# Kernel tuning notes

Hardware: AMD Instinct MI355X
Metric: run time of the kernel (lower is better)

The kernel has to match this reference:

```python
import jax, jax.numpy as jnp
import numpy as np

T, B, E, H, V, L = 64, 64, 512, 1024, 10000, 2


def setup_inputs() -> dict:
    key = jax.random.key(0)
    ks = jax.random.split(key, 24)
    k = 1.0 / np.sqrt(H)
    u = lambda kk, shape, s: jax.random.uniform(kk, shape, jnp.float32, -s, s)
    return {
        "inputs": jax.random.randint(ks[0], (T, B), 0, V, dtype=jnp.int32),
        "hidden": jnp.zeros((L, B, H), jnp.float32),
        "emb": u(ks[1], (V, E), 0.1),
        "Wr0": u(ks[2], (H, E), k),
        "Wz0": u(ks[3], (H, E), k),
        "Wh0": u(ks[4], (H, E), k),
        "WrR": u(ks[5], (L - 1, H, H), k),
        "WzR": u(ks[6], (L - 1, H, H), k),
        "WhR": u(ks[7], (L - 1, H, H), k),
        "brR": u(ks[8], (L - 1, H), k),
        "bzR": u(ks[9], (L - 1, H), k),
        "bhR": u(ks[10], (L - 1, H), k),
        "Ur": u(ks[11], (L, H, H), k),
        "Uz": u(ks[12], (L, H, H), k),
        "Uh": u(ks[13], (L, H, H), k),
        "bur": u(ks[14], (L, H), k),
        "buz": u(ks[15], (L, H), k),
        "buh": u(ks[16], (L, H), k),
        "Wout": u(ks[17], (V, H), 0.1),
        "bout": jnp.zeros((V,), jnp.float32),
    }


def reference(inputs, hidden, emb, Wr0, Wz0, Wh0, WrR, WzR, WhR, brR, bzR, bhR,
              Ur, Uz, Uh, bur, buz, buh, Wout, bout):
    num_layers = hidden.shape[0]
    x_emb = emb[inputs]  # [T, B, E]

    def step(h_prev, x_t):  # h_prev [L,B,H], x_t [B,E]
        x = x_t
        hs = []
        for l in range(num_layers):
            if l == 0:
                rx = x @ Wr0.T  # layer-0 W* have no bias
                zx = x @ Wz0.T
                hx = x @ Wh0.T
            else:
                rx = x @ WrR[l - 1].T + brR[l - 1]
                zx = x @ WzR[l - 1].T + bzR[l - 1]
                hx = x @ WhR[l - 1].T + bhR[l - 1]
            hl = h_prev[l]
            r = jax.nn.sigmoid(rx + hl @ Ur[l].T + bur[l])
            z = jax.nn.sigmoid(zx + hl @ Uz[l].T + buz[l])
            h_tilda = jnp.tanh(hx + (r * hl) @ Uh[l].T + buh[l])
            h_new = (1.0 - z) * hl + z * h_tilda
            hs.append(h_new)
            x = h_new
        logits_t = x @ Wout.T + bout  # [B, V]
        return jnp.stack(hs), logits_t

    h_final, logits = jax.lax.scan(step, hidden, x_emb)
    return logits, h_final  # logits [T,B,V], h_final [L,B,H]
```

## Files before the change

kernel.cpp:

```cpp
#include <hip/hip_runtime.h>
#include <hip/hip_bf16.h>

#define T_ 64
#define B_ 64
#define E_ 512
#define H_ 1024
#define V_ 10000
#define TB 4096
#define BH 65536

typedef unsigned short u16;
typedef unsigned int u32;
typedef unsigned long long u64;
typedef __attribute__((ext_vector_type(8))) short short8v;
typedef __attribute__((ext_vector_type(4))) float f32x4;

__device__ inline f32x4 mfma_bf16(short8v a, short8v b, f32x4 c) {
  return __builtin_amdgcn_mfma_f32_16x16x32_bf16(a, b, c, 0, 0, 0);
}

__device__ inline u16 f2bf(float f) {
  unsigned u = __float_as_uint(f);
  unsigned r = (u + 0x7fffu + ((u >> 16) & 1u)) >> 16;
  return (u16)r;
}
__device__ inline float bf2f(u16 h) { return __uint_as_float(((unsigned)h) << 16); }


__global__ void k_prep(const float* __restrict__ Wr0, const float* __restrict__ Wz0,
                       const float* __restrict__ Wh0, const float* __restrict__ Ur,
                       const float* __restrict__ Uz, const float* __restrict__ Uh,
                       const float* __restrict__ WrR, const float* __restrict__ WzR,
                       const float* __restrict__ WhR, const float* __restrict__ Wout,
                       const int* __restrict__ idx, const float* __restrict__ emb,
                       const float* __restrict__ bur, const float* __restrict__ buz,
                       const float* __restrict__ buh, const float* __restrict__ brR,
                       const float* __restrict__ bzR, const float* __restrict__ bhR,
                       const float* __restrict__ hidden,
                       u16* __restrict__ W0cat, u16* __restrict__ U0cat,
                       u16* __restrict__ U1W, u16* __restrict__ Woutb,
                       u16* __restrict__ x_bf, float* __restrict__ bias0,
                       float* __restrict__ bias1, u16* __restrict__ h0P,
                       u16* __restrict__ h1P) {
  const int HE = H_ * E_;
  const int HH = H_ * H_;
  const size_t n0 = 3u * (size_t)HE;
  const size_t n1 = n0 + 3u * (size_t)HH;
  const size_t n2 = n1 + 3072u * 2048u;
  const size_t n3 = n2 + (size_t)V_ * H_;
  const size_t n4 = n3 + (size_t)TB * E_;
  const size_t n5 = n4 + 3072;
  const size_t n6 = n5 + 65536;
  size_t i = (size_t)blockIdx.x * 256 + threadIdx.x;
  const size_t stride = (size_t)gridDim.x * 256;
  for (; i < n6; i += stride) {
    if (i < n0) {
      int g = (int)(i >> 19), off = (int)(i & (HE - 1));
      const float* s = g == 0 ? Wr0 : (g == 1 ? Wz0 : Wh0);
      W0cat[i] = f2bf(s[off]);
    } else if (i < n1) {
      size_t j = i - n0;
      int g = (int)(j >> 20), off = (int)(j & (HH - 1));
      const float* s = g == 0 ? Ur : (g == 1 ? Uz : Uh);
      U0cat[j] = f2bf(s[off]);
    } else if (i < n2) {
      size_t k = i - n1;
      int row = (int)(k >> 11), kk = (int)(k & 2047);
      int g = row >> 10, jj = row & 1023;
      const float* su = g == 0 ? Ur : (g == 1 ? Uz : Uh);
      const float* sw = g == 0 ? WrR : (g == 1 ? WzR : WhR);
      float v = (kk < 1024) ? su[(size_t)HH + (size_t)jj * 1024 + kk]
                            : sw[(size_t)jj * 1024 + (kk - 1024)];
      U1W[k] = f2bf(v);
    } else if (i < n3) {
      size_t m = i - n2;
      Woutb[m] = f2bf(Wout[m]);
    } else if (i < n4) {
      size_t j = i - n3;
      int row = (int)(j >> 9), e = (int)(j & 511);
      x_bf[j] = f2bf(emb[(size_t)idx[row] * E_ + e]);
    } else if (i < n5) {
      int j = (int)(i - n4);
      int seg = j >> 10, col = j & 1023;
      float b0, b1;
      if (seg == 0)      { b0 = bur[col]; b1 = brR[col] + bur[H_ + col]; }
      else if (seg == 1) { b0 = buz[col]; b1 = bzR[col] + buz[H_ + col]; }
      else               { b0 = buh[col]; b1 = bhR[col] + buh[H_ + col]; }
      bias0[j] = b0; bias1[j] = b1;
    } else {
      int j = (int)(i - n5);
      int row = j >> 10, c = j & 1023;
      int dst = ((c >> 4) << 10) + (row << 4) + (c & 15);
      h0P[dst] = f2bf(hidden[j]);
      h1P[dst] = f2bf(hidden[BH + j]);
    }
  }
}


__global__ __launch_bounds__(256, 2) void k_gemmX(const u16* __restrict__ A,
                                                  const u16* __restrict__ Wt,
                                                  const float* __restrict__ bias,
                                                  u16* __restrict__ XP) {
  const int m0 = blockIdx.x * 128, n0 = blockIdx.y * 128;
  const int wid = threadIdx.x >> 6, lane = threadIdx.x & 63;
  const int wm = wid >> 1, wn = wid & 1;
  const int lrow = lane & 15, lk = (lane >> 4) * 8;
  f32x4 acc[4][4] = {};
  const u16* Ab = A + (size_t)(m0 + wm * 64 + lrow) * 512 + lk;
  const u16* Wb = Wt + (size_t)(n0 + wn * 64 + lrow) * 512 + lk;
  for (int ks = 0; ks < 512; ks += 32) {
    short8v a[4], b[4];
#pragma unroll
    for (int f = 0; f < 4; f++) a[f] = *(const short8v*)(Ab + (size_t)f * 16 * 512 + ks);
#pragma unroll
    for (int f = 0; f < 4; f++) b[f] = *(const short8v*)(Wb + (size_t)f * 16 * 512 + ks);
#pragma unroll
    for (int i = 0; i < 4; i++)
#pragma unroll
      for (int j = 0; j < 4; j++) acc[i][j] = mfma_bf16(a[i], b[j], acc[i][j]);
  }
  const int drow0 = (lane >> 4) * 4, dcol = lane & 15;
#pragma unroll
  for (int i = 0; i < 4; i++)
#pragma unroll
    for (int j = 0; j < 4; j++) {
      int col = n0 + wn * 64 + j * 16 + dcol;
      float bv = bias[col];
      int g = col >> 10, cg = (col & 1023) >> 4, cc = col & 15;
#pragma unroll
      for (int v = 0; v < 4; v++) {
        int row = m0 + wm * 64 + i * 16 + drow0 + v;
        int t = row >> 6, rr = row & 63;
        XP[(((size_t)t * 64 + cg) * 64 + rr) * 48 + g * 16 + cc] = f2bf(acc[i][j][v] + bv);
      }
    }
}


__global__ __launch_bounds__(256, 2) void k_gemmL(const u16* __restrict__ AP,
                                                  const u16* __restrict__ Wt,
                                                  const float* __restrict__ bias,
                                                  float* __restrict__ C) {
  const int xcd = blockIdx.x & 7, idx = blockIdx.x >> 3;
  const int nt = xcd * 10 + (idx % 10);
  const int mt = idx / 10;
  if (nt >= 79) return;
  const int m0 = mt * 128, n0 = nt * 128;
  const int wid = threadIdx.x >> 6, lane = threadIdx.x & 63;
  const int wm = wid >> 1, wn = wid & 1;
  const int lrow = lane & 15, lk = (lane >> 4) * 8;
  const int lkb = lk >> 4, lkc = lk & 15;
  f32x4 acc[4][4] = {};
  const int rowhi = (m0 + wm * 64) >> 6;
  const u16* Ab = AP + (size_t)rowhi * BH + (size_t)lkb * 1024 + lrow * 16 + lkc;
  const u16* Wb = Wt + (size_t)(n0 + wn * 64 + lrow) * 1024 + lk;
  bool nvalid[4];
#pragma unroll
  for (int f = 0; f < 4; f++) nvalid[f] = (n0 + wn * 64 + f * 16 + lrow) < V_;
  const short8v zv = {};
  for (int ks = 0; ks < 1024; ks += 32) {
    short8v a[4], b[4];
#pragma unroll
    for (int f = 0; f < 4; f++) a[f] = *(const short8v*)(Ab + ks * 64 + f * 256);
#pragma unroll
    for (int f = 0; f < 4; f++)
      b[f] = nvalid[f] ? *(const short8v*)(Wb + (size_t)f * 16 * 1024 + ks) : zv;
#pragma unroll
    for (int i = 0; i < 4; i++)
#pragma unroll
      for (int j = 0; j < 4; j++) acc[i][j] = mfma_bf16(a[i], b[j], acc[i][j]);
  }
  const int drow0 = (lane >> 4) * 4, dcol = lane & 15;
#pragma unroll
  for (int i = 0; i < 4; i++)
#pragma unroll
    for (int j = 0; j < 4; j++) {
      int col = n0 + wn * 64 + j * 16 + dcol;
      if (col >= V_) continue;
      float bv = bias[col];
#pragma unroll
      for (int v = 0; v < 4; v++) {
        int row = m0 + wm * 64 + i * 16 + drow0 + v;
        C[(size_t)row * V_ + col] = acc[i][j][v] + bv;
      }
    }
}


__device__ inline void pollall(const int* slots, int tgt) {
  const int lane = threadIdx.x & 63;
  const int* p = slots + lane * 32;
  for (;;) {
    int v = __hip_atomic_load(p, __ATOMIC_RELAXED, __HIP_MEMORY_SCOPE_AGENT);
    if (__all(v >= tgt)) break;
    __builtin_amdgcn_s_sleep(1);
  }
}

__global__ __launch_bounds__(256, 1) void k_recur(
    const u16* __restrict__ U0, const u16* __restrict__ U1W,
    const u16* __restrict__ XP, const float* __restrict__ bias1,
    const float* __restrict__ hidden,
    u16* __restrict__ h0P, u16* __restrict__ h1P,
    u16* __restrict__ r0P, u16* __restrict__ r1P,
    int* __restrict__ flags, float* __restrict__ hfin) {
  __shared__ __align__(16) u16 wlds[65536];

  const int tid = threadIdx.x, gbid = blockIdx.x;
  const int lay = gbid >> 6;
  const int cg = gbid & 63;
  const int jr = cg * 16;
  const int wid = tid >> 6, lane = tid & 63;
  const int lrow = lane & 15, lk = (lane >> 4) * 8;
  const int lk3 = lk >> 3, x7 = lrow & 7;
  const int drow0 = (lane >> 4) * 4, dcol = lane & 15;
  const int abase = (lk >> 4) * 1024 + (wid * 16 + lrow) * 16 + (lk & 15);
  const int KLS = lay ? 11 : 10;
  int* f0s = flags;
  int* f1s = flags + 2048;
  int* myslot = (lay ? f1s : f0s) + cg * 32;

  {
    const u16* Wg = lay ? U1W : U0;
    const int lCPR = lay ? 8 : 7;
    const int NG = lay ? 2 : 3;
    const int total = NG << (4 + lCPR);
    const int KL = 1 << KLS;
    for (int idx = tid; idx < total; idx += 256) {
      int r16 = idx >> lCPR;
      int ch = idx & ((1 << lCPR) - 1);
      int g = r16 >> 4, r = r16 & 15;
      short8v v = *(const short8v*)(Wg + (size_t)((g << 10) + jr + r) * KL + (ch << 3));
      *(short8v*)&wlds[((size_t)r16 << KLS) + ((ch ^ (r & 7)) << 3)] = v;
    }
  }
  __syncthreads();

  const int lbR = lrow << KLS;
  const int lbZ = (16 + lrow) << KLS;
  const int lbH = (32 + lrow) << KLS;
  const u16* Whg = U1W + (size_t)(2048 + jr + lrow) * 2048 + lk;
  const int orow = wid * 16 + drow0;

  float hreg[4];
#pragma unroll
  for (int v = 0; v < 4; v++)
    hreg[v] = hidden[(size_t)lay * BH + (size_t)(orow + v) * 1024 + jr + dcol];

  if (!lay) {
    float xr[4], xz[4], xh[4];
    {
      const u16* xb = XP + (((size_t)0 * 64 + cg) * 64 + orow) * 48 + dcol;
#pragma unroll
      for (int v = 0; v < 4; v++) {
        xr[v] = bf2f(xb[v * 48]);
        xz[v] = bf2f(xb[v * 48 + 16]);
        xh[v] = bf2f(xb[v * 48 + 32]);
      }
    }
    for (int t = 0; t < T_; t++) {
      float zreg[4];
      if (t) { if (wid == 0) pollall(f0s, 2 * t); __syncthreads(); }
      short8v av[32];
      {
        const u16* Ab = h0P + (size_t)t * BH + abase;
#pragma unroll
        for (int i = 0; i < 32; i++) av[i] = *(const short8v*)(Ab + i * 2048);
      }
      f32x4 ar = {};
#pragma unroll
      for (int i = 0; i < 32; i++) {
        const int sw = (((i * 4) + lk3) ^ x7) << 3;
        ar = mfma_bf16(av[i], *(short8v*)&wlds[lbR + sw], ar);
      }
      u16* rtile = r0P + (size_t)t * BH + (size_t)cg * 1024;
#pragma unroll
      for (int v = 0; v < 4; v++) {
        float r = 1.f / (1.f + __expf(-(ar[v] + xr[v])));
        u16 me = f2bf(r * hreg[v]);
        int oth = __shfl_xor((int)me, 1);
        if (!(dcol & 1)) {
          u32 pk = (u32)me | ((u32)(u16)oth << 16);
          __hip_atomic_store((u32*)(rtile + (orow + v) * 16 + dcol), pk,
                             __ATOMIC_RELAXED, __HIP_MEMORY_SCOPE_AGENT);
        }
      }
      asm volatile("s_waitcnt vmcnt(0)" ::: "memory");
      __syncthreads();
      if (tid == 0)
        __hip_atomic_store(myslot, 2 * t + 1, __ATOMIC_RELAXED, __HIP_MEMORY_SCOPE_AGENT);
      f32x4 az = {};
#pragma unroll
      for (int i = 0; i < 32; i++) {
        const int sw = (((i * 4) + lk3) ^ x7) << 3;
        az = mfma_bf16(av[i], *(short8v*)&wlds[lbZ + sw], az);
      }
#pragma unroll
      for (int v = 0; v < 4; v++) zreg[v] = 1.f / (1.f + __expf(-(az[v] + xz[v])));
      float nxr[4], nxz[4], nxh[4];
      {
        int tn = t + 1 < T_ ? t + 1 : T_ - 1;
        const u16* xb = XP + (((size_t)tn * 64 + cg) * 64 + orow) * 48 + dcol;
#pragma unroll
        for (int v = 0; v < 4; v++) {
          nxr[v] = bf2f(xb[v * 48]);
          nxz[v] = bf2f(xb[v * 48 + 16]);
          nxh[v] = bf2f(xb[v * 48 + 32]);
        }
      }
      if (wid == 0) pollall(f0s, 2 * t + 1);
      __syncthreads();
      f32x4 ah = {};
      {
        const u16* Abr = r0P + (size_t)t * BH + abase;
        short8v avr[32];
#pragma unroll
        for (int i = 0; i < 32; i++) avr[i] = *(const short8v*)(Abr + i * 2048);
#pragma unroll
        for (int i = 0; i < 32; i++) {
          const int sw = (((i * 4) + lk3) ^ x7) << 3;
          ah = mfma_bf16(avr[i], *(short8v*)&wlds[lbH + sw], ah);
        }
      }
      u16* htile = h0P + (size_t)(t + 1) * BH + (size_t)cg * 1024;
#pragma unroll
      for (int v = 0; v < 4; v++) {
        float th = tanhf(ah[v] + xh[v]);
        float hn = (1.f - zreg[v]) * hreg[v] + zreg[v] * th;
        hreg[v] = hn;
        u16 me = f2bf(hn);
        int oth = __shfl_xor((int)me, 1);
        if (!(dcol & 1)) {
          u32 pk = (u32)me | ((u32)(u16)oth << 16);
          __hip_atomic_store((u32*)(htile + (orow + v) * 16 + dcol), pk,
                             __ATOMIC_RELAXED, __HIP_MEMORY_SCOPE_AGENT);
        }
        if (t == T_ - 1)
          hfin[(size_t)(orow + v) * 1024 + jr + dcol] = hn;
      }
      asm volatile("s_waitcnt vmcnt(0)" ::: "memory");
      __syncthreads();
      if (tid == 0)
        __hip_atomic_store(myslot, 2 * t + 2, __ATOMIC_RELAXED, __HIP_MEMORY_SCOPE_AGENT);
#pragma unroll
      for (int v = 0; v < 4; v++) { xr[v] = nxr[v]; xz[v] = nxz[v]; xh[v] = nxh[v]; }
    }
  } else {
    float bR = bias1[jr + dcol];
    float bZ = bias1[1024 + jr + dcol];
    float bH = bias1[2048 + jr + dcol];
    if (wid == 0) pollall(f0s, 2);
    __syncthreads();
    for (int t = 0; t < T_; t++) {
      float zreg[4];
      const u16* Ab0 = h0P + (size_t)(t + 1) * BH + abase;
      f32x4 ar = {}, az = {};
      short8v av0[32];
#pragma unroll
      for (int i = 0; i < 32; i++) av0[i] = *(const short8v*)(Ab0 + i * 2048);
#pragma unroll
      for (int i = 0; i < 32; i++) {
        const int sw = ((128 + i * 4 + lk3) ^ x7) << 3;
        ar = mfma_bf16(av0[i], *(short8v*)&wlds[lbR + sw], ar);
        az = mfma_bf16(av0[i], *(short8v*)&wlds[lbZ + sw], az);
      }
      if (wid == 0) {
        if (t) pollall(f1s, 2 * t);
      } else if (wid == 1) {
        int tgt = 2 * (t + 2);
        pollall(f0s, tgt > 2 * T_ ? 2 * T_ : tgt);
      }
      __syncthreads();
      short8v av1[32];
      {
        const u16* Ab1 = h1P + (size_t)t * BH + abase;
#pragma unroll
        for (int i = 0; i < 32; i++) av1[i] = *(const short8v*)(Ab1 + i * 2048);
      }
#pragma unroll
      for (int i = 0; i < 32; i++) {
        const int sw = ((i * 4 + lk3) ^ x7) << 3;
        ar = mfma_bf16(av1[i], *(short8v*)&wlds[lbR + sw], ar);
      }
      u16* rtile = r1P + (size_t)t * BH + (size_t)cg * 1024;
#pragma unroll
      for (int v = 0; v < 4; v++) {
        float r = 1.f / (1.f + __expf(-(ar[v] + bR)));
        u16 me = f2bf(r * hreg[v]);
        int oth = __shfl_xor((int)me, 1);
        if (!(dcol & 1)) {
          u32 pk = (u32)me | ((u32)(u16)oth << 16);
          __hip_atomic_store((u32*)(rtile + (orow + v) * 16 + dcol), pk,
                             __ATOMIC_RELAXED, __HIP_MEMORY_SCOPE_AGENT);
        }
      }
      asm volatile("s_waitcnt vmcnt(0)" ::: "memory");
      __syncthreads();
      if (tid == 0)
        __hip_atomic_store(myslot, 2 * t + 1, __ATOMIC_RELAXED, __HIP_MEMORY_SCOPE_AGENT);
#pragma unroll
      for (int i = 0; i < 32; i++) {
        const int sw = ((i * 4 + lk3) ^ x7) << 3;
        az = mfma_bf16(av1[i], *(short8v*)&wlds[lbZ + sw], az);
      }
#pragma unroll
      for (int v = 0; v < 4; v++) zreg[v] = 1.f / (1.f + __expf(-(az[v] + bZ)));
      f32x4 ah = {};
#pragma unroll
      for (int i = 0; i < 32; i++)
        ah = mfma_bf16(av0[i], *(const short8v*)(Whg + 1024 + i * 32), ah);
      if (wid == 0) pollall(f1s, 2 * t + 1);
      __syncthreads();
      {
        const u16* Abr = r1P + (size_t)t * BH + abase;
        short8v avr[32];
#pragma unroll
        for (int i = 0; i < 32; i++) avr[i] = *(const short8v*)(Abr + i * 2048);
#pragma unroll
        for (int i = 0; i < 32; i++)
          ah = mfma_bf16(avr[i], *(const short8v*)(Whg + i * 32), ah);
      }
      u16* htile = h1P + (size_t)(t + 1) * BH + (size_t)cg * 1024;
#pragma unroll
      for (int v = 0; v < 4; v++) {
        float th = tanhf(ah[v] + bH);
        float hn = (1.f - zreg[v]) * hreg[v] + zreg[v] * th;
        hreg[v] = hn;
        u16 me = f2bf(hn);
        int oth = __shfl_xor((int)me, 1);
        if (!(dcol & 1)) {
          u32 pk = (u32)me | ((u32)(u16)oth << 16);
          __hip_atomic_store((u32*)(htile + (orow + v) * 16 + dcol), pk,
                             __ATOMIC_RELAXED, __HIP_MEMORY_SCOPE_AGENT);
        }
        if (t == T_ - 1)
          hfin[(size_t)BH + (size_t)(orow + v) * 1024 + jr + dcol] = hn;
      }
      asm volatile("s_waitcnt vmcnt(0)" ::: "memory");
      __syncthreads();
      if (tid == 0)
        __hip_atomic_store(myslot, 2 * t + 2, __ATOMIC_RELAXED, __HIP_MEMORY_SCOPE_AGENT);
    }
  }
}


extern "C" void kernel_launch(void* const* d_in, const int* in_sizes, int n_in,
                              void* d_out, int out_size, void* d_ws, size_t ws_size,
                              hipStream_t stream) {
  const int* inputs = (const int*)d_in[0];
  const float* hidden = (const float*)d_in[1];
  const float* emb = (const float*)d_in[2];
  const float* Wr0 = (const float*)d_in[3];
  const float* Wz0 = (const float*)d_in[4];
  const float* Wh0 = (const float*)d_in[5];
  const float* WrR = (const float*)d_in[6];
  const float* WzR = (const float*)d_in[7];
  const float* WhR = (const float*)d_in[8];
  const float* brR = (const float*)d_in[9];
  const float* bzR = (const float*)d_in[10];
  const float* bhR = (const float*)d_in[11];
  const float* Ur = (const float*)d_in[12];
  const float* Uz = (const float*)d_in[13];
  const float* Uh = (const float*)d_in[14];
  const float* bur = (const float*)d_in[15];
  const float* buz = (const float*)d_in[16];
  const float* buh = (const float*)d_in[17];
  const float* Wout = (const float*)d_in[18];
  const float* bout = (const float*)d_in[19];
  float* out = (float*)d_out;

  char* ws = (char*)d_ws;
  size_t off = 0;
  auto alloc = [&](size_t bytes) -> void* {
    void* p = ws + off;
    off += (bytes + 255) & ~(size_t)255;
    return p;
  };
  u16* x_bf  = (u16*)alloc((size_t)TB * E_ * 2);
  u16* W0cat = (u16*)alloc((size_t)3072 * 512 * 2);
  u16* U0cat = (u16*)alloc((size_t)3072 * 1024 * 2);
  u16* U1W   = (u16*)alloc((size_t)3072 * 2048 * 2);
  u16* Woutb = (u16*)alloc((size_t)V_ * H_ * 2);
  float* bias0 = (float*)alloc(3072 * 4);
  float* bias1 = (float*)alloc(3072 * 4);
  u16* XP    = (u16*)alloc((size_t)TB * 3072 * 2);
  u16* h0P   = (u16*)alloc((size_t)(T_ + 1) * BH * 2);
  u16* h1P   = (u16*)alloc((size_t)(T_ + 1) * BH * 2);
  u16* r0P   = (u16*)alloc((size_t)T_ * BH * 2);
  u16* r1P   = (u16*)alloc((size_t)T_ * BH * 2);
  int* flags = (int*)alloc(32768);
  (void)ws_size; (void)in_sizes; (void)n_in; (void)out_size;

  hipMemsetAsync(flags, 0, 32768, stream);

  k_prep<<<2048, 256, 0, stream>>>(Wr0, Wz0, Wh0, Ur, Uz, Uh, WrR, WzR, WhR, Wout,
                                   inputs, emb, bur, buz, buh, brR, bzR, bhR, hidden,
                                   W0cat, U0cat, U1W, Woutb, x_bf, bias0, bias1,
                                   h0P, h1P);
  k_gemmX<<<dim3(32, 24), 256, 0, stream>>>(x_bf, W0cat, bias0, XP);
  k_recur<<<128, 256, 0, stream>>>(U0cat, U1W, XP, bias1, hidden, h0P, h1P,
                                   r0P, r1P, flags, out + (size_t)TB * V_);
  k_gemmL<<<2560, 256, 0, stream>>>(h1P + BH, Woutb, bout, out);
}
```

Before: 1.382 ms.

## Fuse output projection GEMM into recurrent kernel with flag-gated tiles

Removes the separate output-logits GEMM launch and appends its tiles as extra blocks of the persistent recurrence kernel. Each GEMM block polls the layer-1 progress flags until the two timesteps covering its 128 rows are finished, then computes them, so the vocabulary projection overlaps the sequential recurrence. The added blocks share the device with the 128 recurrence blocks, which rely on co-residency for their spin-wait barriers. This risks scheduling or deadlock issues if GEMM blocks take the slots the recurrence blocks need, and their polling and memory traffic may slow the critical path.

```diff
diff --git a/kernel.cpp b/kernel.cpp
--- a/kernel.cpp
+++ b/kernel.cpp
@@ -138,63 +138,14 @@
 }
 
 
-__global__ __launch_bounds__(256, 2) void k_gemmL(const u16* __restrict__ AP,
-                                                  const u16* __restrict__ Wt,
-                                                  const float* __restrict__ bias,
-                                                  float* __restrict__ C) {
-  const int xcd = blockIdx.x & 7, idx = blockIdx.x >> 3;
-  const int nt = xcd * 10 + (idx % 10);
-  const int mt = idx / 10;
-  if (nt >= 79) return;
-  const int m0 = mt * 128, n0 = nt * 128;
-  const int wid = threadIdx.x >> 6, lane = threadIdx.x & 63;
-  const int wm = wid >> 1, wn = wid & 1;
-  const int lrow = lane & 15, lk = (lane >> 4) * 8;
-  const int lkb = lk >> 4, lkc = lk & 15;
-  f32x4 acc[4][4] = {};
-  const int rowhi = (m0 + wm * 64) >> 6;
-  const u16* Ab = AP + (size_t)rowhi * BH + (size_t)lkb * 1024 + lrow * 16 + lkc;
-  const u16* Wb = Wt + (size_t)(n0 + wn * 64 + lrow) * 1024 + lk;
-  bool nvalid[4];
-#pragma unroll
-  for (int f = 0; f < 4; f++) nvalid[f] = (n0 + wn * 64 + f * 16 + lrow) < V_;
-  const short8v zv = {};
-  for (int ks = 0; ks < 1024; ks += 32) {
-    short8v a[4], b[4];
-#pragma unroll
-    for (int f = 0; f < 4; f++) a[f] = *(const short8v*)(Ab + ks * 64 + f * 256);
-#pragma unroll
-    for (int f = 0; f < 4; f++)
-      b[f] = nvalid[f] ? *(const short8v*)(Wb + (size_t)f * 16 * 1024 + ks) : zv;
-#pragma unroll
-    for (int i = 0; i < 4; i++)
-#pragma unroll
-      for (int j = 0; j < 4; j++) acc[i][j] = mfma_bf16(a[i], b[j], acc[i][j]);
-  }
-  const int drow0 = (lane >> 4) * 4, dcol = lane & 15;
-#pragma unroll
-  for (int i = 0; i < 4; i++)
-#pragma unroll
-    for (int j = 0; j < 4; j++) {
-      int col = n0 + wn * 64 + j * 16 + dcol;
-      if (col >= V_) continue;
-      float bv = bias[col];
-#pragma unroll
-      for (int v = 0; v < 4; v++) {
-        int row = m0 + wm * 64 + i * 16 + drow0 + v;
-        C[(size_t)row * V_ + col] = acc[i][j][v] + bv;
-      }
-    }
-}
-
-
+template <int SLP>
 __device__ inline void pollall(const int* slots, int tgt) {
   const int lane = threadIdx.x & 63;
   const int* p = slots + lane * 32;
   for (;;) {
     int v = __hip_atomic_load(p, __ATOMIC_RELAXED, __HIP_MEMORY_SCOPE_AGENT);
     if (__all(v >= tgt)) break;
-    __builtin_amdgcn_s_sleep(1);
+    __builtin_amdgcn_s_sleep(SLP);
   }
 }
 
@@ -204,21 +155,72 @@
     const float* __restrict__ hidden,
     u16* __restrict__ h0P, u16* __restrict__ h1P,
     u16* __restrict__ r0P, u16* __restrict__ r1P,
+    const u16* __restrict__ Woutb, const float* __restrict__ bout,
+    float* __restrict__ out,
     int* __restrict__ flags, float* __restrict__ hfin) {
   __shared__ __align__(16) u16 wlds[65536];
 
   const int tid = threadIdx.x, gbid = blockIdx.x;
+  const int wid = tid >> 6, lane = tid & 63;
+  const int lrow = lane & 15, lk = (lane >> 4) * 8;
+  const int drow0 = (lane >> 4) * 4, dcol = lane & 15;
+  int* f0s = flags;
+  int* f1s = flags + 2048;
+
+  if (gbid >= 128) {
+    const int w = gbid - 128;
+    const int mt = w / 79, nt = w % 79;
+    const int m0 = mt * 128, n0 = nt * 128;
+    const int wm = wid >> 1, wn = wid & 1;
+    const int lkb = lk >> 4, lkc = lk & 15;
+    if (wid == 0) {
+      int tgt = 4 * mt + 4;
+      pollall<32>(f1s, tgt > 2 * T_ ? 2 * T_ : tgt);
+    }
+    __syncthreads();
+    const u16* AP = h1P + BH;
+    f32x4 acc[4][4] = {};
+    const int rowhi = (m0 + wm * 64) >> 6;
+    const u16* Ab = AP + (size_t)rowhi * BH + (size_t)lkb * 1024 + lrow * 16 + lkc;
+    const u16* Wb = Woutb + (size_t)(n0 + wn * 64 + lrow) * 1024 + lk;
+    bool nvalid[4];
+#pragma unroll
+    for (int f = 0; f < 4; f++) nvalid[f] = (n0 + wn * 64 + f * 16 + lrow) < V_;
+    const short8v zv = {};
+    for (int ks = 0; ks < 1024; ks += 32) {
+      short8v a[4], b[4];
+#pragma unroll
+      for (int f = 0; f < 4; f++) a[f] = *(const short8v*)(Ab + ks * 64 + f * 256);
+#pragma unroll
+      for (int f = 0; f < 4; f++)
+        b[f] = nvalid[f] ? *(const short8v*)(Wb + (size_t)f * 16 * 1024 + ks) : zv;
+#pragma unroll
+      for (int i = 0; i < 4; i++)
+#pragma unroll
+        for (int j = 0; j < 4; j++) acc[i][j] = mfma_bf16(a[i], b[j], acc[i][j]);
+    }
+#pragma unroll
+    for (int i = 0; i < 4; i++)
+#pragma unroll
+      for (int j = 0; j < 4; j++) {
+        int col = n0 + wn * 64 + j * 16 + dcol;
+        if (col >= V_) continue;
+        float bv = bout[col];
+#pragma unroll
+        for (int v = 0; v < 4; v++) {
+          int row = m0 + wm * 64 + i * 16 + drow0 + v;
+          out[(size_t)row * V_ + col] = acc[i][j][v] + bv;
+        }
+      }
+    return;
+  }
+
   const int lay = gbid >> 6;
   const int cg = gbid & 63;
   const int jr = cg * 16;
-  const int wid = tid >> 6, lane = tid & 63;
-  const int lrow = lane & 15, lk = (lane >> 4) * 8;
   const int lk3 = lk >> 3, x7 = lrow & 7;
-  const int drow0 = (lane >> 4) * 4, dcol = lane & 15;
   const int abase = (lk >> 4) * 1024 + (wid * 16 + lrow) * 16 + (lk & 15);
   const int KLS = lay ? 11 : 10;
-  int* f0s = flags;
-  int* f1s = flags + 2048;
   int* myslot = (lay ? f1s : f0s) + cg * 32;
 
   {
@@ -261,7 +263,7 @@
     }
     for (int t = 0; t < T_; t++) {
       float zreg[4];
-      if (t) { if (wid == 0) pollall(f0s, 2 * t); __syncthreads(); }
+      if (t) { if (wid == 0) pollall<1>(f0s, 2 * t); __syncthreads(); }
       short8v av[32];
       {
         const u16* Ab = h0P + (size_t)t * BH + abase;
@@ -309,7 +311,7 @@
           nxh[v] = bf2f(xb[v * 48 + 32]);
         }
       }
-      if (wid == 0) pollall(f0s, 2 * t + 1);
+      if (wid == 0) pollall<1>(f0s, 2 * t + 1);
       __syncthreads();
       f32x4 ah = {};
       {
@@ -350,7 +352,7 @@
     float bR = bias1[jr + dcol];
     float bZ = bias1[1024 + jr + dcol];
     float bH = bias1[2048 + jr + dcol];
-    if (wid == 0) pollall(f0s, 2);
+    if (wid == 0) pollall<1>(f0s, 2);
     __syncthreads();
     for (int t = 0; t < T_; t++) {
       float zreg[4];
@@ -366,10 +368,10 @@
         az = mfma_bf16(av0[i], *(short8v*)&wlds[lbZ + sw], az);
       }
       if (wid == 0) {
-        if (t) pollall(f1s, 2 * t);
+        if (t) pollall<1>(f1s, 2 * t);
       } else if (wid == 1) {
         int tgt = 2 * (t + 2);
-        pollall(f0s, tgt > 2 * T_ ? 2 * T_ : tgt);
+        pollall<1>(f0s, tgt > 2 * T_ ? 2 * T_ : tgt);
       }
       __syncthreads();
       short8v av1[32];
@@ -410,7 +412,7 @@
 #pragma unroll
       for (int i = 0; i < 32; i++)
         ah = mfma_bf16(av0[i], *(const short8v*)(Whg + 1024 + i * 32), ah);
-      if (wid == 0) pollall(f1s, 2 * t + 1);
+      if (wid == 0) pollall<1>(f1s, 2 * t + 1);
       __syncthreads();
       {
         const u16* Abr = r1P + (size_t)t * BH + abase;
@@ -493,14 +495,14 @@
   int* flags = (int*)alloc(32768);
   (void)ws_size; (void)in_sizes; (void)n_in; (void)out_size;
 
-  hipMemsetAsync(flags, 0, 32768, stream);
+  (void)hipMemsetAsync(flags, 0, 32768, stream);
 
   k_prep<<<2048, 256, 0, stream>>>(Wr0, Wz0, Wh0, Ur, Uz, Uh, WrR, WzR, WhR, Wout,
                                    inputs, emb, bur, buz, buh, brR, bzR, bhR, hidden,
                                    W0cat, U0cat, U1W, Woutb, x_bf, bias0, bias1,
                                    h0P, h1P);
   k_gemmX<<<dim3(32, 24), 256, 0, stream>>>(x_bf, W0cat, bias0, XP);
-  k_recur<<<128, 256, 0, stream>>>(U0cat, U1W, XP, bias1, hidden, h0P, h1P,
-                                   r0P, r1P, flags, out + (size_t)TB * V_);
-  k_gemmL<<<2560, 256, 0, stream>>>(h1P + BH, Woutb, bout, out);
-}
+  k_recur<<<128 + 32 * 79, 256, 0, stream>>>(U0cat, U1W, XP, bias1, hidden, h0P, h1P,
+                                             r0P, r1P, Woutb, bout, out, flags,
+                                             out + (size_t)TB * V_);
+}
```

New measurement: 1.269 ms. -8.2%, faster.
